# Performance work log

Measured on AMD Instinct MI355X. Metric: run time of the kernel, lower is better.

## Reference

```python
import jax, jax.numpy as jnp
import numpy as np
import math

B, N, D = 2, 4096, 1024
NUM_LAYERS = 12
INIT_RANGE = 0.02


def setup_inputs() -> dict:
    key = jax.random.key(0)
    k1, k2 = jax.random.split(key)
    hidden_states = jax.random.normal(k1, (B, N, D), dtype=jnp.float32)
    std = INIT_RANGE / math.sqrt(2.0 * NUM_LAYERS * D)
    queries = jax.random.normal(k2, (D, D), dtype=jnp.float32) * std
    return {"hidden_states": hidden_states, "queries": queries}


def reference(hidden_states, queries):
    # Q = F.linear(X, W) = X @ W^T  -> [B, N, D]
    q = jnp.einsum('bnd,ed->bne', hidden_states, queries)
    # pre_attn = Q @ X^T  -> [B, N, N]
    pre_attn = jnp.einsum('bne,bme->bnm', q, hidden_states)
    # attention = pre_attn @ X  -> [B, N, D]
    attention = jnp.einsum('bnm,bmd->bnd', pre_attn, hidden_states)
    return attention
```

## Files before the change

kernel.cpp:

```cpp
#include <hip/hip_runtime.h>
#include <hip/hip_bf16.h>
#include <stdint.h>

using bf16 = __hip_bfloat16;
typedef __attribute__((ext_vector_type(8))) short short8;
typedef __attribute__((ext_vector_type(4))) float f32x4;

#define BM 128
#define BK 32

__device__ __forceinline__ void g2lds16(const void* g, void* l) {
    __builtin_amdgcn_global_load_lds(
        (const __attribute__((address_space(1))) void*)g,
        (__attribute__((address_space(3))) void*)l,
        16, 0, 0);
}

template <int N>
__device__ __forceinline__ void s_wait_vmcnt() {
    asm volatile("s_waitcnt vmcnt(%0)" :: "n"(N) : "memory");
}

__device__ __forceinline__ short f2bs(float x) {
    union { bf16 h; short s; } u;
    u.h = __float2bfloat16(x);
    return u.s;
}

__device__ __forceinline__ int bswz(int row, int cg) { return cg ^ ((row >> 1) & 3); }
__device__ __forceinline__ int fswz(int row, int cg) { return cg ^ (row & 7); }

__global__ __launch_bounds__(256)
void transpose_cvt(const float* __restrict__ src, ushort* __restrict__ dstT,
                   ushort* __restrict__ dstN,
                   int R, int C, long sstride, long dstrideT, long dstrideN)
{
    __shared__ __align__(16) ushort t[64][72];
    const float* s = src + (size_t)blockIdx.z * sstride;
    ushort*      dT = dstT + (size_t)blockIdx.z * dstrideT;
    const int r0 = blockIdx.y * 64, c0 = blockIdx.x * 64;
    const int tid = threadIdx.x;
#pragma unroll
    for (int ii = 0; ii < 4; ++ii) {
        int idx = ii * 256 + tid;
        int r = idx >> 4, c4 = (idx & 15) * 4;
        float4 v = *(const float4*)&s[(size_t)(r0 + r) * C + c0 + c4];
        union { ushort u[4]; uint2 q; } o;
        o.u[0] = (ushort)f2bs(v.x); o.u[1] = (ushort)f2bs(v.y);
        o.u[2] = (ushort)f2bs(v.z); o.u[3] = (ushort)f2bs(v.w);
        *(uint2*)&t[r][c4] = o.q;
        if (dstN) {
            ushort* dN = dstN + (size_t)blockIdx.z * dstrideN;
            *(uint2*)&dN[(size_t)(r0 + r) * C + c0 + c4] = o.q;
        }
    }
    __syncthreads();
#pragma unroll
    for (int ii = 0; ii < 2; ++ii) {
        int idx = ii * 256 + tid;
        int c = idx >> 3, r8 = (idx & 7) * 8;
        union { ushort u[8]; uint4 v; } tmp;
#pragma unroll
        for (int j = 0; j < 8; ++j) tmp.u[j] = t[r8 + j][c];
        *(uint4*)&dT[(size_t)(c0 + c) * R + r0 + r8] = tmp.v;
    }
}

__global__ __launch_bounds__(256)
void cvt_f32_bf16(const float* __restrict__ in, ushort* __restrict__ out, int n4)
{
    int i = blockIdx.x * 256 + threadIdx.x;
    if (i >= n4) return;
    float4 v = ((const float4*)in)[i];
    union { ushort u[4]; uint2 q; } o;
    o.u[0] = (ushort)f2bs(v.x); o.u[1] = (ushort)f2bs(v.y);
    o.u[2] = (ushort)f2bs(v.z); o.u[3] = (ushort)f2bs(v.w);
    ((uint2*)out)[i] = o.q;
}

template <int MODE, int A_F32, int NFRAG>
__global__ __launch_bounds__(256)
void gemm_bt(const void* __restrict__ Av, const bf16* __restrict__ B,
             void* __restrict__ Cv, int M, int N, int K, int kChunks,
             long sA, long sB, long sC)
{
    constexpr int BN  = 32 * NFRAG;
    constexpr int BSH = (BN * BK * 2) / (256 * 16);
    constexpr int ASH = A_F32 ? 4 : 2;
    constexpr int L   = ASH + BSH;
    constexpr int ANE = BM * BK * (A_F32 ? 2 : 1);
    constexpr int BNE = BN * BK;
    __shared__ __align__(16) bf16 lA[3][ANE];
    __shared__ __align__(16) bf16 lB[3][BNE];

    const int z     = blockIdx.z;
    const int batch = z / kChunks;
    const int chunk = z - batch * kChunks;
    const int kLen  = K / kChunks;
    const int k0    = chunk * kLen;

    const int gx  = gridDim.x;
    int flat = blockIdx.y * gx + blockIdx.x;
    const int cpx = (gx * gridDim.y) >> 3;
    flat = (flat & 7) * cpx + (flat >> 3);
    const int m0 = (flat / gx) * BM;
    const int n0 = (flat - (flat / gx) * gx) * BN;

    const int tid  = threadIdx.x;
    const int lane = tid & 63;
    const int wave = tid >> 6;
    const int wr   = wave >> 1, wc = wave & 1;
    const int ml   = lane & 15;
    const int q    = lane >> 4;

    const bf16* Bb = B + (size_t)batch * sB;
    const bf16* bp[BSH];
#pragma unroll
    for (int s = 0; s < BSH; ++s) {
        int idx = s * 256 + tid;
        int row = idx >> 2, cg = idx & 3;
        bp[s] = Bb + (size_t)(n0 + row) * K + k0 + 8 * bswz(row, cg);
    }

    const float* a32[4];
    const bf16*  a16[2];
    if constexpr (A_F32) {
        const float* Ab = (const float*)Av + (size_t)batch * sA;
#pragma unroll
        for (int s = 0; s < 4; ++s) {
            int idx = s * 256 + tid;
            int row = idx >> 3, cg = idx & 7;
            a32[s] = Ab + (size_t)(m0 + row) * K + k0 + 4 * fswz(row, cg);
        }
    } else {
        const bf16* Ab = (const bf16*)Av + (size_t)batch * sA;
#pragma unroll
        for (int s = 0; s < 2; ++s) {
            int idx = s * 256 + tid;
            int row = idx >> 2, cg = idx & 3;
            a16[s] = Ab + (size_t)(m0 + row) * K + k0 + 8 * bswz(row, cg);
        }
    }

    f32x4 acc[4][NFRAG] = {};

    auto stage = [&](int buf) {
        if constexpr (A_F32) {
            float* lAf = (float*)lA[buf];
#pragma unroll
            for (int s = 0; s < 4; ++s) {
                g2lds16(a32[s], &lAf[(s * 256 + tid) * 4]);
                a32[s] += BK;
            }
        } else {
#pragma unroll
            for (int s = 0; s < 2; ++s) {
                g2lds16(a16[s], &lA[buf][(s * 256 + tid) * 8]);
                a16[s] += BK;
            }
        }
#pragma unroll
        for (int s = 0; s < BSH; ++s) {
            g2lds16(bp[s], &lB[buf][(s * 256 + tid) * 8]);
            bp[s] += BK;
        }
    };

    auto frags = [&](int buf, short8 (&af)[4], short8 (&bfr)[NFRAG]) {
        const bf16* cA = lA[buf];
        const bf16* cB = lB[buf];
#pragma unroll
        for (int i = 0; i < 4; ++i) {
            const int rA = wr * 64 + i * 16 + ml;
            if constexpr (A_F32) {
                const float* lAf = (const float*)cA;
                float4 x0 = *(const float4*)&lAf[rA * 32 + 4 * fswz(rA, 2 * q)];
                float4 x1 = *(const float4*)&lAf[rA * 32 + 4 * fswz(rA, 2 * q + 1)];
                af[i][0] = f2bs(x0.x); af[i][1] = f2bs(x0.y);
                af[i][2] = f2bs(x0.z); af[i][3] = f2bs(x0.w);
                af[i][4] = f2bs(x1.x); af[i][5] = f2bs(x1.y);
                af[i][6] = f2bs(x1.z); af[i][7] = f2bs(x1.w);
            } else {
                af[i] = *(const short8*)&cA[rA * 32 + 8 * bswz(rA, q)];
            }
        }
#pragma unroll
        for (int j = 0; j < NFRAG; ++j) {
            const int rB = wc * (16 * NFRAG) + j * 16 + ml;
            bfr[j] = *(const short8*)&cB[rB * 32 + 8 * bswz(rB, q)];
        }
    };

    auto mfma = [&](short8 (&af)[4], short8 (&bfr)[NFRAG]) {
#pragma unroll
        for (int mi = 0; mi < 4; ++mi)
#pragma unroll
            for (int nj = 0; nj < NFRAG; ++nj)
                acc[mi][nj] = __builtin_amdgcn_mfma_f32_16x16x32_bf16(
                    af[mi], bfr[nj], acc[mi][nj], 0, 0, 0);
    };

    const int nk = kLen / BK;
    stage(0); stage(1);
    int cur = 0;
    for (int t = 0; t < nk - 2; ++t) {
        s_wait_vmcnt<L>();
        __builtin_amdgcn_s_barrier();
        short8 af_[4], bf_[NFRAG];
        frags(cur, af_, bf_);
        int nb = cur + 2; nb = (nb >= 3) ? nb - 3 : nb;
        stage(nb);
        mfma(af_, bf_);
        asm volatile("s_waitcnt lgkmcnt(0)" ::: "memory");
        cur = (cur == 2) ? 0 : cur + 1;
    }
    {
        s_wait_vmcnt<L>();
        __builtin_amdgcn_s_barrier();
        short8 af_[4], bf_[NFRAG];
        frags(cur, af_, bf_);
        mfma(af_, bf_);
        cur = (cur == 2) ? 0 : cur + 1;
    }
    {
        s_wait_vmcnt<0>();
        __builtin_amdgcn_s_barrier();
        short8 af_[4], bf_[NFRAG];
        frags(cur, af_, bf_);
        mfma(af_, bf_);
    }

#pragma unroll
    for (int mi = 0; mi < 4; ++mi)
#pragma unroll
        for (int nj = 0; nj < NFRAG; ++nj)
#pragma unroll
            for (int r = 0; r < 4; ++r) {
                int row = m0 + wr * 64 + mi * 16 + q * 4 + r;
                int col = n0 + wc * (16 * NFRAG) + nj * 16 + ml;
                if constexpr (MODE == 1) {
                    float* Cf = (float*)Cv + (size_t)batch * sC;
                    atomicAdd(&Cf[(size_t)row * N + col], acc[mi][nj][r]);
                } else if constexpr (MODE == 0) {
                    ushort* Cb = (ushort*)Cv + (size_t)batch * sC;
                    Cb[(size_t)row * N + col] = (ushort)f2bs(acc[mi][nj][r]);
                } else {
                    float* Cf = (float*)Cv + (size_t)batch * sC;
                    Cf[(size_t)row * N + col] = acc[mi][nj][r];
                }
            }
}

extern "C" void kernel_launch(void* const* d_in, const int* in_sizes, int n_in,
                              void* d_out, int out_size, void* d_ws, size_t ws_size,
                              hipStream_t stream)
{
    const int B = 2, N = 4096, D = 1024;
    const float* X = (const float*)d_in[0];
    const float* W = (const float*)d_in[1];
    float* out = (float*)d_out;

    char* ob = (char*)d_out;
    char* ws = (char*)d_ws;
    ushort* Xt  = (ushort*)ob;
    float*  Mtf = (float*)ob;
    float*  Gf  = (float*)(ob + (16ll << 20));
    ushort* Wt  = (ushort*)(ob + (28ll << 20));

    const bool bigws = ws_size >= (20ull << 20);
    ushort* Xb = bigws ? (ushort*)ws : nullptr;
    ushort* Mt = (ushort*)(ws + (bigws ? (16ll << 20) : 0));

    transpose_cvt<<<dim3(D / 64, N / 64, B), 256, 0, stream>>>(
        X, Xt, Xb, N, D, (long)N * D, (long)D * N, (long)N * D);
    transpose_cvt<<<dim3(D / 64, D / 64, 1), 256, 0, stream>>>(
        W, Wt, nullptr, D, D, 0, 0, 0);
    (void)hipMemsetAsync(Gf, 0, (size_t)B * D * D * sizeof(float), stream);
    gemm_bt<1, 0, 2><<<dim3(D / 64, D / BM, B * 4), 256, 0, stream>>>(
        (const void*)Xt, (const bf16*)Xt, Gf, D, D, N, 4,
        (long)D * N, (long)D * N, (long)D * D);
    (void)hipMemsetAsync(Mtf, 0, (size_t)B * D * D * sizeof(float), stream);
    gemm_bt<1, 1, 2><<<dim3(D / 64, D / BM, B * 2), 256, 0, stream>>>(
        (const void*)Gf, (const bf16*)Wt, Mtf, D, D, D, 2,
        (long)D * D, 0, (long)D * D);
    cvt_f32_bf16<<<dim3((B * D * D / 4 + 255) / 256), 256, 0, stream>>>(
        Mtf, Mt, B * D * D / 4);
    if (bigws) {
        gemm_bt<2, 0, 2><<<dim3(D / 64, N / BM, B), 256, 0, stream>>>(
            (const void*)Xb, (const bf16*)Mt, out, N, D, D, 1,
            (long)N * D, (long)D * D, (long)N * D);
    } else {
        gemm_bt<2, 1, 2><<<dim3(D / 64, N / BM, B), 256, 0, stream>>>(
            (const void*)X, (const bf16*)Mt, out, N, D, D, 1,
            (long)N * D, (long)D * D, (long)N * D);
    }
}
```

Baseline: 202.2 us.

## Drop split-K and bf16 conversion for second GEMM, widen tiles, remap workgroups

Result: faster. 175.4 us (-13.2%).

```diff
diff --git a/kernel.cpp b/kernel.cpp
--- a/kernel.cpp
+++ b/kernel.cpp
@@ -64,18 +64,6 @@
         for (int j = 0; j < 8; ++j) tmp.u[j] = t[r8 + j][c];
         *(uint4*)&dT[(size_t)(c0 + c) * R + r0 + r8] = tmp.v;
     }
-}
-
-__global__ __launch_bounds__(256)
-void cvt_f32_bf16(const float* __restrict__ in, ushort* __restrict__ out, int n4)
-{
-    int i = blockIdx.x * 256 + threadIdx.x;
-    if (i >= n4) return;
-    float4 v = ((const float4*)in)[i];
-    union { ushort u[4]; uint2 q; } o;
-    o.u[0] = (ushort)f2bs(v.x); o.u[1] = (ushort)f2bs(v.y);
-    o.u[2] = (ushort)f2bs(v.z); o.u[3] = (ushort)f2bs(v.w);
-    ((uint2*)out)[i] = o.q;
 }
 
 template <int MODE, int A_F32, int NFRAG>
@@ -93,18 +81,21 @@
     __shared__ __align__(16) bf16 lA[3][ANE];
     __shared__ __align__(16) bf16 lB[3][BNE];
 
-    const int z     = blockIdx.z;
+    const int gx   = gridDim.x, gy = gridDim.y;
+    const int nwg  = gx * gy * gridDim.z;
+    const int wgid = (blockIdx.z * gy + blockIdx.y) * gx + blockIdx.x;
+    const int lid  = (wgid & 7) * (nwg >> 3) + (wgid >> 3);
+    const int pz   = gx * gy;
+    const int z    = lid / pz;
+    const int rem  = lid - z * pz;
+    const int my   = rem / gx;
+    const int m0   = my * BM;
+    const int n0   = (rem - my * gx) * BN;
+
     const int batch = z / kChunks;
     const int chunk = z - batch * kChunks;
     const int kLen  = K / kChunks;
     const int k0    = chunk * kLen;
-
-    const int gx  = gridDim.x;
-    int flat = blockIdx.y * gx + blockIdx.x;
-    const int cpx = (gx * gridDim.y) >> 3;
-    flat = (flat & 7) * cpx + (flat >> 3);
-    const int m0 = (flat / gx) * BM;
-    const int n0 = (flat - (flat / gx) * gx) * BN;
 
     const int tid  = threadIdx.x;
     const int lane = tid & 63;
@@ -262,10 +253,9 @@
 
     char* ob = (char*)d_out;
     char* ws = (char*)d_ws;
-    ushort* Xt  = (ushort*)ob;
-    float*  Mtf = (float*)ob;
-    float*  Gf  = (float*)(ob + (16ll << 20));
-    ushort* Wt  = (ushort*)(ob + (28ll << 20));
+    ushort* Xt = (ushort*)ob;
+    float*  Gf = (float*)(ob + (16ll << 20));
+    ushort* Wt = (ushort*)(ob + (28ll << 20));
 
     const bool bigws = ws_size >= (20ull << 20);
     ushort* Xb = bigws ? (ushort*)ws : nullptr;
@@ -276,21 +266,18 @@
     transpose_cvt<<<dim3(D / 64, D / 64, 1), 256, 0, stream>>>(
         W, Wt, nullptr, D, D, 0, 0, 0);
     (void)hipMemsetAsync(Gf, 0, (size_t)B * D * D * sizeof(float), stream);
-    gemm_bt<1, 0, 2><<<dim3(D / 64, D / BM, B * 4), 256, 0, stream>>>(
+    gemm_bt<1, 0, 4><<<dim3(D / 128, D / BM, B * 4), 256, 0, stream>>>(
         (const void*)Xt, (const bf16*)Xt, Gf, D, D, N, 4,
         (long)D * N, (long)D * N, (long)D * D);
-    (void)hipMemsetAsync(Mtf, 0, (size_t)B * D * D * sizeof(float), stream);
-    gemm_bt<1, 1, 2><<<dim3(D / 64, D / BM, B * 2), 256, 0, stream>>>(
-        (const void*)Gf, (const bf16*)Wt, Mtf, D, D, D, 2,
+    gemm_bt<0, 1, 2><<<dim3(D / 64, D / BM, B), 256, 0, stream>>>(
+        (const void*)Gf, (const bf16*)Wt, Mt, D, D, D, 1,
         (long)D * D, 0, (long)D * D);
-    cvt_f32_bf16<<<dim3((B * D * D / 4 + 255) / 256), 256, 0, stream>>>(
-        Mtf, Mt, B * D * D / 4);
     if (bigws) {
-        gemm_bt<2, 0, 2><<<dim3(D / 64, N / BM, B), 256, 0, stream>>>(
+        gemm_bt<2, 0, 4><<<dim3(D / 128, N / BM, B), 256, 0, stream>>>(
             (const void*)Xb, (const bf16*)Mt, out, N, D, D, 1,
             (long)N * D, (long)D * D, (long)N * D);
     } else {
-        gemm_bt<2, 1, 2><<<dim3(D / 64, N / BM, B), 256, 0, stream>>>(
+        gemm_bt<2, 1, 4><<<dim3(D / 128, N / BM, B), 256, 0, stream>>>(
             (const void*)X, (const bf16*)Mt, out, N, D, D, 1,
             (long)N * D, (long)D * D, (long)N * D);
     }
```
